# Kernel tuning notes

Hardware: AMD Instinct MI355X
Metric: run time of the kernel (lower is better)

Reference implementation:

```python
import jax, jax.numpy as jnp
import numpy as np
import math

H = 12   # num_attention_heads
DH = 64  # attention_head_size
HID = H * DH  # 768


def setup_inputs() -> dict:
    key = jax.random.key(0)
    ks = jax.random.split(key, 16)
    B, S = 2, 128
    inp = {
        'hidden_states': jax.random.normal(ks[0], (B, S, HID), jnp.float32),
        'attention_mask': jnp.zeros((B, 1, 1, S), jnp.float32),
        'inference_path': jax.random.normal(ks[1], (B, S, S, HID), jnp.float32),
        'span_mask': jax.random.uniform(ks[2], (B, 1, S, S), jnp.float32),
    }
    sc = 1.0 / math.sqrt(HID)
    # weights stored as [in, out]; y = x @ W + b
    inp['Wq'] = jax.random.normal(ks[3], (HID, HID), jnp.float32) * sc
    inp['bq'] = jnp.zeros((HID,), jnp.float32)
    inp['Wk'] = jax.random.normal(ks[4], (HID, HID), jnp.float32) * sc
    inp['bk'] = jnp.zeros((HID,), jnp.float32)
    inp['Wv'] = jax.random.normal(ks[5], (HID, HID), jnp.float32) * sc
    inp['bv'] = jnp.zeros((HID,), jnp.float32)
    inp['Wpv'] = jax.random.normal(ks[6], (HID, DH), jnp.float32) * sc
    inp['bpv'] = jnp.zeros((DH,), jnp.float32)
    inp['Wip'] = jax.random.normal(ks[7], (HID, 2 * HID), jnp.float32) * sc
    inp['Wmlp'] = jax.random.normal(ks[8], (HID + DH, HID), jnp.float32) * sc
    inp['bmlp'] = jnp.zeros((HID,), jnp.float32)
    return inp


def reference(hidden_states, attention_mask, inference_path, span_mask,
              Wq, bq, Wk, bk, Wv, bv, Wpv, bpv, Wip, Wmlp, bmlp):
    B, S, _ = hidden_states.shape
    # projections
    q = (hidden_states @ Wq + bq).reshape(B, S, H, DH).transpose(0, 2, 1, 3)  # [B,H,S,Dh]
    k = (hidden_states @ Wk + bk).reshape(B, S, H, DH).transpose(0, 2, 1, 3)
    v = (hidden_states @ Wv + bv).reshape(B, S, H, DH).transpose(0, 2, 1, 3)
    # parse value path: [B,1,S,Dh]
    pv = (hidden_states @ Wpv + bpv).reshape(B, S, 1, DH).transpose(0, 2, 1, 3)
    parse_ctx = jnp.matmul(span_mask, pv)              # [B,1,S,Dh]
    parse_ctx = parse_ctx.transpose(0, 2, 1, 3)        # [B,S,1,Dh]
    # relative inference-path bias: raw view (matches torch .view semantics)
    ip = inference_path @ Wip                           # [B,S,S,2*HID]
    ra, rb = jnp.split(ip, 2, axis=-1)                  # each [B,S,S,HID]
    ra = ra.reshape(B, H, S, S, DH)
    rb = rb.reshape(B, H, S, S, DH)
    qe = q[:, :, :, None, :] + ra                       # [B,H,S,S,Dh]
    ke = k[:, :, None, :, :] + rb                       # [B,H,S,S,Dh]
    scores = jnp.einsum('bhqkd,bhqkd->bhqk', qe, ke)
    scores = scores / math.sqrt(DH) + attention_mask
    probs = jax.nn.softmax(scores, axis=-1)             # dropout is identity in eval
    ctx = jnp.matmul(probs, v)                          # [B,H,S,Dh]
    ctx = ctx.transpose(0, 2, 1, 3)                     # [B,S,H,Dh]
    ctx = jnp.concatenate([ctx, parse_ctx], axis=-2)    # [B,S,H+1,Dh]
    ctx = ctx.reshape(B, S, HID + DH)
    return ctx @ Wmlp + bmlp                            # [B,S,HID]
```

## Files before the change

kernel.cpp:

```cpp
#include <hip/hip_runtime.h>
#include <hip/hip_bf16.h>


typedef __attribute__((ext_vector_type(8))) __bf16 bf16x8;
typedef __attribute__((ext_vector_type(16))) float f32x16;

#define QKV_OFF   0u
#define ARENA_OFF 2424832u
#define SC_OFF    4784128u
#define CTX_OFF   6356992u

__global__ __launch_bounds__(256)
void prep_kernel(const float* __restrict__ Wip, __bf16* __restrict__ arena) {
  const int l = threadIdx.x & 63;
  const int f = blockIdx.x * 4 + (threadIdx.x >> 6);
  const int n32 = f / 48, k16 = f - n32 * 48;
  const float* src = Wip + (size_t)(k16 * 16 + (l >> 5) * 8) * 1536 + n32 * 32 + (l & 31);
  union { __bf16 h[8]; uint4 u; } pk;
#pragma unroll
  for (int j = 0; j < 8; j++) pk.h[j] = (__bf16)src[(size_t)j * 1536];
  ((uint4*)arena)[(size_t)f * 64 + l] = pk.u;
}

__global__ __launch_bounds__(64)
void proj_kernel(const float* __restrict__ hs,
                 const float* __restrict__ Wq, const float* __restrict__ bq,
                 const float* __restrict__ Wk, const float* __restrict__ bk,
                 const float* __restrict__ Wv, const float* __restrict__ bv,
                 const float* __restrict__ Wpv, const float* __restrict__ bpv,
                 float* __restrict__ qkv) {
  const int n0 = blockIdx.x * 32;
  const int m0 = blockIdx.y * 32;
  const float* W; const float* bias; int noff, ldw;
  if (n0 < 768)       { W = Wq;  bias = bq;  noff = n0;        ldw = 768; }
  else if (n0 < 1536) { W = Wk;  bias = bk;  noff = n0 - 768;  ldw = 768; }
  else if (n0 < 2304) { W = Wv;  bias = bv;  noff = n0 - 1536; ldw = 768; }
  else                { W = Wpv; bias = bpv; noff = n0 - 2304; ldw = 64;  }
  const int l = threadIdx.x;
  const int rsel = l & 31, ksel = l >> 5;
  f32x16 acc;
#pragma unroll
  for (int z = 0; z < 16; z++) acc[z] = 0.f;

#pragma unroll 4
  for (int k16 = 0; k16 < 48; k16++) {
    const float* ap = hs + (size_t)(m0 + rsel) * 768 + k16 * 16 + ksel * 8;
    float4 a0 = *(const float4*)ap;
    float4 a1 = *(const float4*)(ap + 4);
    union { __bf16 h[8]; bf16x8 v; } pa;
    pa.h[0] = (__bf16)a0.x; pa.h[1] = (__bf16)a0.y; pa.h[2] = (__bf16)a0.z; pa.h[3] = (__bf16)a0.w;
    pa.h[4] = (__bf16)a1.x; pa.h[5] = (__bf16)a1.y; pa.h[6] = (__bf16)a1.z; pa.h[7] = (__bf16)a1.w;
    const float* bp = W + (size_t)(k16 * 16 + ksel * 8) * ldw + noff + rsel;
    union { __bf16 h[8]; bf16x8 v; } pb;
#pragma unroll
    for (int j = 0; j < 8; j++) pb.h[j] = (__bf16)bp[(size_t)j * ldw];
    acc = __builtin_amdgcn_mfma_f32_32x32x16_bf16(pa.v, pb.v, acc, 0, 0, 0);
  }
#pragma unroll
  for (int reg = 0; reg < 16; reg++) {
    int row = (reg & 3) + ((reg >> 2) << 3) + (ksel << 2);
    qkv[(size_t)(m0 + row) * 2368 + n0 + rsel] = acc[reg] + bias[noff + rsel];
  }
}

extern __shared__ char smem_raw[];

__global__ __launch_bounds__(512, 2)
void score_kernel(const float* __restrict__ infp,
                  const __bf16* __restrict__ arena,
                  const float* __restrict__ qkv,
                  float* __restrict__ scores) {
  char* Abase = smem_raw;
  float* lds_sc = (float*)(smem_raw + 99840);
  const int tid = threadIdx.x;
  const int lane = tid & 63;
  const int ml = lane & 31;
  const int kh = lane >> 5;
  const int wv = tid >> 6;
  const int wc = wv & 3;
  const int wd = wv >> 2;
  const int blk = blockIdx.x;
  const int b = blk >> 8;
  const int r0 = (blk & 255) << 6;

  for (int z = tid; z < 768; z += 512) lds_sc[z] = 0.f;

  const uint4* BA = (const uint4*)arena;
  const uint4* bptr  = BA + (size_t)((2 * wc + wd) * 48) * 64 + lane;
  const uint4* bptr2 = bptr + 73728;
  uint4 B0[8], B1[8];
  bf16x8 AfA[8], AfB[8];
  f32x16 acc_ra[2], acc_rb[2];

  auto loadB = [&](uint4* dst) {
#pragma unroll
    for (int ks = 0; ks < 4; ks++) {
      dst[ks * 2]     = bptr[ks * 64];
      dst[ks * 2 + 1] = bptr2[ks * 64];
    }
  };

  loadB(B0);
  bptr += 256; bptr2 += 256;

  {
    const float4* A4 = (const float4*)(infp + (size_t)(b * 16384 + r0) * 768);
#pragma unroll
    for (int p = 0; p < 12; p++) {
      int idx = p * 512 + tid;
      int m = (int)(((unsigned)idx * 10923u) >> 20);
      int g = idx - m * 96;
      float4 v0 = A4[m * 192 + g * 2];
      float4 v1 = A4[m * 192 + g * 2 + 1];
      union { __bf16 h[8]; uint4 u; } pk;
      pk.h[0] = (__bf16)v0.x; pk.h[1] = (__bf16)v0.y;
      pk.h[2] = (__bf16)v0.z; pk.h[3] = (__bf16)v0.w;
      pk.h[4] = (__bf16)v1.x; pk.h[5] = (__bf16)v1.y;
      pk.h[6] = (__bf16)v1.z; pk.h[7] = (__bf16)v1.w;
      int F = (m >> 5) * 48 + (g >> 1);
      int slot = (m & 31) + ((g & 1) << 5);
      *(uint4*)(Abase + ((F * 65 + slot) << 4)) = pk.u;
    }
  }
  __syncthreads();

  const size_t lane_off = (size_t)(lane << 4);
  int aoff = 0;
  auto loadA = [&](bf16x8* bank) {
    const char* ab = Abase + lane_off + aoff;
#pragma unroll
    for (int mt = 0; mt < 2; mt++)
#pragma unroll
      for (int ks = 0; ks < 4; ks++)
        bank[mt * 4 + ks] = *(const bf16x8*)(ab + mt * 49920 + ks * 1040);
  };
  auto mfma_step = [&](const bf16x8* Af, const uint4* Bb) {
#pragma unroll
    for (int ks = 0; ks < 4; ks++) {
      bf16x8 bra = *(const bf16x8*)&Bb[ks * 2];
      bf16x8 brb = *(const bf16x8*)&Bb[ks * 2 + 1];
#pragma unroll
      for (int mt = 0; mt < 2; mt++) {
        acc_ra[mt] = __builtin_amdgcn_mfma_f32_32x32x16_bf16(Af[mt * 4 + ks], bra, acc_ra[mt], 0, 0, 0);
        acc_rb[mt] = __builtin_amdgcn_mfma_f32_32x32x16_bf16(Af[mt * 4 + ks], brb, acc_rb[mt], 0, 0, 0);
      }
    }
  };
  auto epilogue = [&](int c) {
    int d = wd * 32 + ml;
#pragma unroll
    for (int mt = 0; mt < 2; mt++) {
      float qv[16], kv[16];
#pragma unroll
      for (int reg = 0; reg < 16; reg++) {
        int row = mt * 32 + (reg & 3) + ((reg >> 2) << 3) + (kh << 2);
        int t = 12 * (r0 + row) + c;
        int hh = t >> 14;
        int ii = (t >> 7) & 127;
        int jj = t & 127;
        qv[reg] = qkv[(size_t)((b << 7) + ii) * 2368 + (hh << 6) + d];
        kv[reg] = qkv[(size_t)((b << 7) + jj) * 2368 + 768 + (hh << 6) + d];
      }
#pragma unroll
      for (int reg = 0; reg < 16; reg++) {
        int row = mt * 32 + (reg & 3) + ((reg >> 2) << 3) + (kh << 2);
        float p = (qv[reg] + acc_ra[mt][reg]) * (kv[reg] + acc_rb[mt][reg]);
        p += __shfl_xor(p, 16);
        p += __shfl_xor(p, 8);
        p += __shfl_xor(p, 4);
        p += __shfl_xor(p, 2);
        p += __shfl_xor(p, 1);
        if (ml == 0) atomicAdd(&lds_sc[row * 12 + c], p);
      }
    }
#pragma unroll
    for (int mt = 0; mt < 2; mt++)
#pragma unroll
      for (int z = 0; z < 16; z++) { acc_ra[mt][z] = 0.f; acc_rb[mt][z] = 0.f; }
  };

#pragma unroll
  for (int mt = 0; mt < 2; mt++)
#pragma unroll
    for (int z = 0; z < 16; z++) { acc_ra[mt][z] = 0.f; acc_rb[mt][z] = 0.f; }

  loadA(AfA);
  aoff = 4160;

  int kc = 0, c = wc;
#pragma unroll 1
  for (int ith = 0; ith < 18; ith++) {
    {
      int kcn = kc + 1, cn = c;
      if (kcn == 12) { kcn = 0; cn = c + 4; }
      loadB(B1);
      if (kcn == 11) { bptr += 21760; bptr2 += 21760; } else { bptr += 256; bptr2 += 256; }
      loadA(AfB);
      aoff = (kcn == 11) ? 0 : aoff + 4160;
      mfma_step(AfA, B0);
      kc = kcn; c = cn;
    }
    {
      int kcn = kc + 1, cn = c;
      if (kcn == 12) { kcn = 0; cn = c + 4; }
      if (ith < 17) {
        loadB(B0);
        if (kcn == 11) { bptr += 21760; bptr2 += 21760; } else { bptr += 256; bptr2 += 256; }
        loadA(AfA);
        aoff = (kcn == 11) ? 0 : aoff + 4160;
      }
      mfma_step(AfB, B1);
      if (kc == 11) epilogue(c);
      kc = kcn; c = cn;
    }
  }

  __syncthreads();
  for (int z = tid; z < 768; z += 512) {
    int row = z / 12;
    int cc = z - row * 12;
    int t = 12 * (r0 + row) + cc;
    int hh = t >> 14;
    int ii = (t >> 7) & 127;
    int jj = t & 127;
    scores[(size_t)((b * 12 + hh) * 128 + ii) * 128 + jj] = lds_sc[z];
  }
}

__global__ __launch_bounds__(256)
void attn_kernel(const float* __restrict__ scores, const float* __restrict__ qkv,
                 const float* __restrict__ mask, const float* __restrict__ span,
                 float* __restrict__ ctx) {
  const int i = blockIdx.x;
  const int b = blockIdx.y;
  const int tid = threadIdx.x;
  const int l = tid & 63;
  const int wvi = tid >> 6;
  __shared__ float w[13][132];
  for (int r = wvi; r < 13; r += 4) {
    if (r < 12) {
      const float* sp = scores + (size_t)((b * 12 + r) * 128 + i) * 128;
      float s0 = sp[l] * 0.125f + mask[b * 128 + l];
      float s1 = sp[l + 64] * 0.125f + mask[b * 128 + l + 64];
      float mx = fmaxf(s0, s1);
#pragma unroll
      for (int o = 32; o; o >>= 1) mx = fmaxf(mx, __shfl_xor(mx, o));
      float e0 = __expf(s0 - mx), e1 = __expf(s1 - mx);
      float sm = e0 + e1;
#pragma unroll
      for (int o = 32; o; o >>= 1) sm += __shfl_xor(sm, o);
      float inv = 1.f / sm;
      w[r][l] = e0 * inv;
      w[r][l + 64] = e1 * inv;
    } else {
      const float* sp = span + (size_t)(b * 128 + i) * 128;
      w[12][l] = sp[l];
      w[12][l + 64] = sp[l + 64];
    }
  }
  __syncthreads();
  for (int o = tid; o < 832; o += 256) {
    int h = o >> 6, d = o & 63;
    const float* vp = qkv + (size_t)(b * 128) * 2368 + (h < 12 ? 1536 + h * 64 : 2304) + d;
    float acc = 0.f;
#pragma unroll 8
    for (int j = 0; j < 128; j++) acc += w[h][j] * vp[(size_t)j * 2368];
    ctx[(size_t)(b * 128 + i) * 832 + o] = acc;
  }
}

__global__ __launch_bounds__(64)
void out_kernel(const float* __restrict__ ctxb, const float* __restrict__ Wmlp,
                const float* __restrict__ bmlp, float* __restrict__ out) {
  const int n0 = blockIdx.x * 32;
  const int m0 = blockIdx.y * 32;
  const int l = threadIdx.x;
  const int rsel = l & 31, ksel = l >> 5;
  f32x16 acc;
#pragma unroll
  for (int z = 0; z < 16; z++) acc[z] = 0.f;

#pragma unroll 4
  for (int k16 = 0; k16 < 52; k16++) {
    const float* ap = ctxb + (size_t)(m0 + rsel) * 832 + k16 * 16 + ksel * 8;
    float4 a0 = *(const float4*)ap;
    float4 a1 = *(const float4*)(ap + 4);
    union { __bf16 h[8]; bf16x8 v; } pa;
    pa.h[0] = (__bf16)a0.x; pa.h[1] = (__bf16)a0.y; pa.h[2] = (__bf16)a0.z; pa.h[3] = (__bf16)a0.w;
    pa.h[4] = (__bf16)a1.x; pa.h[5] = (__bf16)a1.y; pa.h[6] = (__bf16)a1.z; pa.h[7] = (__bf16)a1.w;
    const float* bp = Wmlp + (size_t)(k16 * 16 + ksel * 8) * 768 + n0 + rsel;
    union { __bf16 h[8]; bf16x8 v; } pb;
#pragma unroll
    for (int j = 0; j < 8; j++) pb.h[j] = (__bf16)bp[(size_t)j * 768];
    acc = __builtin_amdgcn_mfma_f32_32x32x16_bf16(pa.v, pb.v, acc, 0, 0, 0);
  }
#pragma unroll
  for (int reg = 0; reg < 16; reg++) {
    int row = (reg & 3) + ((reg >> 2) << 3) + (ksel << 2);
    out[(size_t)(m0 + row) * 768 + n0 + rsel] = acc[reg] + bmlp[n0 + rsel];
  }
}

extern "C" void kernel_launch(void* const* d_in, const int* in_sizes, int n_in,
                              void* d_out, int out_size, void* d_ws, size_t ws_size,
                              hipStream_t stream) {
  const float* hs   = (const float*)d_in[0];
  const float* mask = (const float*)d_in[1];
  const float* infp = (const float*)d_in[2];
  const float* span = (const float*)d_in[3];
  const float* Wq   = (const float*)d_in[4];
  const float* bq   = (const float*)d_in[5];
  const float* Wk   = (const float*)d_in[6];
  const float* bk   = (const float*)d_in[7];
  const float* Wv   = (const float*)d_in[8];
  const float* bv   = (const float*)d_in[9];
  const float* Wpv  = (const float*)d_in[10];
  const float* bpv  = (const float*)d_in[11];
  const float* Wip  = (const float*)d_in[12];
  const float* Wmlp = (const float*)d_in[13];
  const float* bmlp = (const float*)d_in[14];
  float* out = (float*)d_out;

  char* ws = (char*)d_ws;
  float*  qkv    = (float*)(ws + QKV_OFF);
  __bf16* arena  = (__bf16*)(ws + ARENA_OFF);
  float*  scores = (float*)(ws + SC_OFF);
  float*  ctx    = (float*)(ws + CTX_OFF);

  prep_kernel<<<dim3(576), 256, 0, stream>>>(Wip, arena);
  proj_kernel<<<dim3(74, 8), 64, 0, stream>>>(hs, Wq, bq, Wk, bk, Wv, bv, Wpv, bpv, qkv);
  score_kernel<<<dim3(512), 512, 102912, stream>>>(infp, arena, qkv, scores);
  attn_kernel<<<dim3(128, 2), 256, 0, stream>>>(scores, qkv, mask, span, ctx);
  out_kernel<<<dim3(24, 8), 64, 0, stream>>>(ctx, Wmlp, bmlp, out);
}
```

Measured before the change: 371.0 us.

## Triple-buffer B fragments, single-buffer A, nontemporal loads for inference path

The main GEMM loop moves from double-buffering both A (LDS) and B (global) fragments to triple-buffering the global B weight fragments, which gives each global load two MFMA steps of latency slack. The A fragments are now loaded from LDS into a single register bank right before use. The inference_path staging loads switch to nontemporal loads so the large streamed input does not pollute the cache. This trades B-side register pressure and exposed LDS latency for deeper global prefetch.

```diff
diff --git a/kernel.cpp b/kernel.cpp
--- a/kernel.cpp
+++ b/kernel.cpp
@@ -4,6 +4,7 @@
 
 typedef __attribute__((ext_vector_type(8))) __bf16 bf16x8;
 typedef __attribute__((ext_vector_type(16))) float f32x16;
+typedef __attribute__((ext_vector_type(4))) float f32x4;
 
 #define QKV_OFF   0u
 #define ARENA_OFF 2424832u
@@ -88,8 +89,9 @@
   const uint4* BA = (const uint4*)arena;
   const uint4* bptr  = BA + (size_t)((2 * wc + wd) * 48) * 64 + lane;
   const uint4* bptr2 = bptr + 73728;
-  uint4 B0[8], B1[8];
-  bf16x8 AfA[8], AfB[8];
+  int kpn = 0;
+  uint4 B0[8], B1[8], B2[8];
+  bf16x8 Af[8];
   f32x16 acc_ra[2], acc_rb[2];
 
   auto loadB = [&](uint4* dst) {
@@ -98,25 +100,27 @@
       dst[ks * 2]     = bptr[ks * 64];
       dst[ks * 2 + 1] = bptr2[ks * 64];
     }
+    if (kpn == 11) { bptr += 21760; bptr2 += 21760; kpn = 0; }
+    else           { bptr += 256;   bptr2 += 256;   kpn++;  }
   };
 
   loadB(B0);
-  bptr += 256; bptr2 += 256;
+  loadB(B1);
 
   {
-    const float4* A4 = (const float4*)(infp + (size_t)(b * 16384 + r0) * 768);
+    const f32x4* A4 = (const f32x4*)(infp + (size_t)(b * 16384 + r0) * 768);
 #pragma unroll
     for (int p = 0; p < 12; p++) {
       int idx = p * 512 + tid;
       int m = (int)(((unsigned)idx * 10923u) >> 20);
       int g = idx - m * 96;
-      float4 v0 = A4[m * 192 + g * 2];
-      float4 v1 = A4[m * 192 + g * 2 + 1];
+      f32x4 v0 = __builtin_nontemporal_load(A4 + m * 192 + g * 2);
+      f32x4 v1 = __builtin_nontemporal_load(A4 + m * 192 + g * 2 + 1);
       union { __bf16 h[8]; uint4 u; } pk;
-      pk.h[0] = (__bf16)v0.x; pk.h[1] = (__bf16)v0.y;
-      pk.h[2] = (__bf16)v0.z; pk.h[3] = (__bf16)v0.w;
-      pk.h[4] = (__bf16)v1.x; pk.h[5] = (__bf16)v1.y;
-      pk.h[6] = (__bf16)v1.z; pk.h[7] = (__bf16)v1.w;
+      pk.h[0] = (__bf16)v0[0]; pk.h[1] = (__bf16)v0[1];
+      pk.h[2] = (__bf16)v0[2]; pk.h[3] = (__bf16)v0[3];
+      pk.h[4] = (__bf16)v1[0]; pk.h[5] = (__bf16)v1[1];
+      pk.h[6] = (__bf16)v1[2]; pk.h[7] = (__bf16)v1[3];
       int F = (m >> 5) * 48 + (g >> 1);
       int slot = (m & 31) + ((g & 1) << 5);
       *(uint4*)(Abase + ((F * 65 + slot) << 4)) = pk.u;
@@ -125,16 +129,15 @@
   __syncthreads();
 
   const size_t lane_off = (size_t)(lane << 4);
-  int aoff = 0;
-  auto loadA = [&](bf16x8* bank) {
-    const char* ab = Abase + lane_off + aoff;
+  auto loadA = [&](int kcc) {
+    const char* ab = Abase + lane_off + kcc * 4160;
 #pragma unroll
     for (int mt = 0; mt < 2; mt++)
 #pragma unroll
       for (int ks = 0; ks < 4; ks++)
-        bank[mt * 4 + ks] = *(const bf16x8*)(ab + mt * 49920 + ks * 1040);
+        Af[mt * 4 + ks] = *(const bf16x8*)(ab + mt * 49920 + ks * 1040);
   };
-  auto mfma_step = [&](const bf16x8* Af, const uint4* Bb) {
+  auto mfma_step = [&](const uint4* Bb) {
 #pragma unroll
     for (int ks = 0; ks < 4; ks++) {
       bf16x8 bra = *(const bf16x8*)&Bb[ks * 2];
@@ -184,42 +187,34 @@
 #pragma unroll
     for (int z = 0; z < 16; z++) { acc_ra[mt][z] = 0.f; acc_rb[mt][z] = 0.f; }
 
-  loadA(AfA);
-  aoff = 4160;
-
-  int kc = 0, c = wc;
+  int kcc = 0, cc = wc;
 #pragma unroll 1
-  for (int ith = 0; ith < 18; ith++) {
+  for (int it = 0; it < 12; it++) {
     {
-      int kcn = kc + 1, cn = c;
-      if (kcn == 12) { kcn = 0; cn = c + 4; }
-      loadB(B1);
-      if (kcn == 11) { bptr += 21760; bptr2 += 21760; } else { bptr += 256; bptr2 += 256; }
-      loadA(AfB);
-      aoff = (kcn == 11) ? 0 : aoff + 4160;
-      mfma_step(AfA, B0);
-      kc = kcn; c = cn;
+      loadB(B2);
+      loadA(kcc);
+      mfma_step(B0);
+      if (kcc == 11) { epilogue(cc); kcc = 0; cc += 4; } else kcc++;
     }
     {
-      int kcn = kc + 1, cn = c;
-      if (kcn == 12) { kcn = 0; cn = c + 4; }
-      if (ith < 17) {
-        loadB(B0);
-        if (kcn == 11) { bptr += 21760; bptr2 += 21760; } else { bptr += 256; bptr2 += 256; }
-        loadA(AfA);
-        aoff = (kcn == 11) ? 0 : aoff + 4160;
-      }
-      mfma_step(AfB, B1);
-      if (kc == 11) epilogue(c);
-      kc = kcn; c = cn;
+      if (it < 11) loadB(B0);
+      loadA(kcc);
+      mfma_step(B1);
+      if (kcc == 11) { epilogue(cc); kcc = 0; cc += 4; } else kcc++;
+    }
+    {
+      if (it < 11) loadB(B1);
+      loadA(kcc);
+      mfma_step(B2);
+      if (kcc == 11) { epilogue(cc); kcc = 0; cc += 4; } else kcc++;
     }
   }
 
   __syncthreads();
   for (int z = tid; z < 768; z += 512) {
     int row = z / 12;
-    int cc = z - row * 12;
-    int t = 12 * (r0 + row) + cc;
+    int ccc = z - row * 12;
+    int t = 12 * (r0 + row) + ccc;
     int hh = t >> 14;
     int ii = (t >> 7) & 127;
     int jj = t & 127;
```

Measured after the change: 354.3 us. 1.05x faster.
